# Performance work log

Measured on AMD Instinct MI355X. Metric: run time of the kernel, lower is better.

The kernel has to match this reference:

```python
import jax, jax.numpy as jnp
import numpy as np

EMBED_DIM = 1024
NUM_HEADS = 16
HEAD_DIM = EMBED_DIM // NUM_HEADS


def setup_inputs() -> dict:
    key = jax.random.key(0)
    k_x, k_wqkv, k_bqkv, k_wp, k_bp = jax.random.split(key, 5)
    B, S = 4, 2048
    scale = 1.0 / np.sqrt(EMBED_DIM)
    return {
        "x": jax.random.normal(k_x, (B, S, EMBED_DIM), dtype=jnp.float32),
        # torch nn.Linear stores weight as [out_features, in_features]
        "w_qkv": jax.random.uniform(k_wqkv, (3 * EMBED_DIM, EMBED_DIM), dtype=jnp.float32, minval=-scale, maxval=scale),
        "b_qkv": jax.random.uniform(k_bqkv, (3 * EMBED_DIM,), dtype=jnp.float32, minval=-scale, maxval=scale),
        "w_proj": jax.random.uniform(k_wp, (EMBED_DIM, EMBED_DIM), dtype=jnp.float32, minval=-scale, maxval=scale),
        "b_proj": jax.random.uniform(k_bp, (EMBED_DIM,), dtype=jnp.float32, minval=-scale, maxval=scale),
    }


def reference(x, w_qkv, b_qkv, w_proj, b_proj):
    B, S, _ = x.shape
    # qkv projection: [B,S,3E]
    qkv = jnp.einsum('bse,fe->bsf', x, w_qkv) + b_qkv
    qkv = qkv.reshape(B, S, 3, NUM_HEADS, HEAD_DIM)
    qkv = jnp.transpose(qkv, (2, 0, 3, 1, 4))  # [3,B,H,S,Dh]
    q, k, v = qkv[0], qkv[1], qkv[2]
    # scaled dot-product attention (no mask, eval-mode dropout = identity)
    scores = jnp.einsum('bhqd,bhkd->bhqk', q, k) / np.sqrt(HEAD_DIM)
    attn = jax.nn.softmax(scores, axis=-1)
    out = jnp.einsum('bhqk,bhkd->bhqd', attn, v)  # [B,H,S,Dh]
    out = jnp.transpose(out, (0, 2, 1, 3)).reshape(B, S, EMBED_DIM)
    return jnp.einsum('bse,fe->bsf', out, w_proj) + b_proj
```

## Files before the change

kernel.cpp:

```cpp
#include <hip/hip_runtime.h>

#define EDIM 1024
#define NHEADS 16
#define HDIM 64
#define SEQ 2048
#define BATCH 4
#define MROWS (BATCH * SEQ)
#define NQKV (3 * EDIM)
#define QKB 2048

typedef __attribute__((ext_vector_type(4))) float f32x4;
typedef __attribute__((ext_vector_type(8))) short s16x8;
typedef __attribute__((ext_vector_type(4))) short s16x4;
typedef __attribute__((ext_vector_type(4))) unsigned int u32x4;

#define AS1 __attribute__((address_space(1)))
#define AS3 __attribute__((address_space(3)))
#define GLOAD_LDS16(g, l) __builtin_amdgcn_global_load_lds( \
    (AS1 void*)(void*)(g), (AS3 void*)(void*)(l), 16, 0, 0)

static __device__ __forceinline__ unsigned short f2bf(float f) {
  unsigned int u = __builtin_bit_cast(unsigned int, f);
  u += 0x7fffu + ((u >> 16) & 1u);
  return (unsigned short)(u >> 16);
}

static __device__ __forceinline__ float fexp2(float x) {
  float r;
  asm("v_exp_f32 %0, %1" : "=v"(r) : "v"(x));
  return r;
}

static __device__ __forceinline__ unsigned int cvtpk(float a, float b) {
  unsigned int r;
  asm("v_cvt_pk_bf16_f32 %0, %1, %2" : "=v"(r) : "v"(a), "v"(b));
  return r;
}

static __device__ __forceinline__ f32x4 mfma_bf16(s16x8 a, s16x8 b, f32x4 c) {
  return __builtin_amdgcn_mfma_f32_16x16x32_bf16(a, b, c, 0, 0, 0);
}

__global__ void __launch_bounds__(256) cvt_all(const float* __restrict__ x,
                                               const float* __restrict__ wq,
                                               const float* __restrict__ wp,
                                               unsigned short* __restrict__ out) {
  const int i = blockIdx.x * 256 + threadIdx.x;
  const float* src;
  int j;
  if (i < 2097152) { src = x;  j = i; }
  else if (i < 2883584) { src = wq; j = i - 2097152; }
  else { src = wp; j = i - 2883584; }
  const float4 v = ((const float4*)src)[j];
  ushort4 o;
  o.x = f2bf(v.x); o.y = f2bf(v.y); o.z = f2bf(v.z); o.w = f2bf(v.w);
  ((ushort4*)out)[i] = o;
}

template <int MODE>
__global__ void __launch_bounds__(256) gemm_bt(const unsigned short* __restrict__ A,
                                               const unsigned short* __restrict__ B,
                                               const float* __restrict__ bias,
                                               void* __restrict__ Cout,
                                               int M, int N, int K) {
  __shared__ unsigned short As[128 * 32];
  __shared__ unsigned short Bs[128 * 32];
  const int tid = threadIdx.x;
  const int lane = tid & 63;
  const int wave = tid >> 6;
  const int wr = wave >> 1, wc = wave & 1;
  const int lr = lane & 15, kg = lane >> 4;

  const long m0 = (long)blockIdx.x * 128;
  const long n0 = (long)blockIdx.y * 128;

  f32x4 acc[4][4] = {};

  for (int kt = 0; kt < K; kt += 32) {
#pragma unroll
    for (int i = 0; i < 2; ++i) {
      const int c = wave + i * 4;
      const int slot = c * 64 + lane;
      const int row = slot >> 2;
      const int col = (slot & 3) << 3;
      GLOAD_LDS16(A + (m0 + row) * K + kt + col, &As[c * 512]);
      GLOAD_LDS16(B + (n0 + row) * K + kt + col, &Bs[c * 512]);
    }
    __syncthreads();

    s16x8 af[4], bf[4];
#pragma unroll
    for (int mt = 0; mt < 4; ++mt)
      af[mt] = *(const s16x8*)&As[(wr * 64 + mt * 16 + lr) * 32 + kg * 8];
#pragma unroll
    for (int nt = 0; nt < 4; ++nt)
      bf[nt] = *(const s16x8*)&Bs[(wc * 64 + nt * 16 + lr) * 32 + kg * 8];
#pragma unroll
    for (int mt = 0; mt < 4; ++mt)
#pragma unroll
      for (int nt = 0; nt < 4; ++nt)
        acc[mt][nt] = mfma_bf16(af[mt], bf[nt], acc[mt][nt]);
    __syncthreads();
  }

#pragma unroll
  for (int nt = 0; nt < 4; ++nt) {
    const long col = n0 + wc * 64 + nt * 16 + lr;
    const float bv = (MODE == 2) ? 0.f : bias[col];
#pragma unroll
    for (int mt = 0; mt < 4; ++mt) {
#pragma unroll
      for (int r = 0; r < 4; ++r) {
        const long row = m0 + wr * 64 + mt * 16 + kg * 4 + r;
        if (MODE == 0) {
          float v = acc[mt][nt][r] + bv;
          if (col < EDIM) v *= 0.18033688011112042f;
          ((unsigned short*)Cout)[row * N + col] = f2bf(v);
        } else if (MODE == 1) {
          ((float*)Cout)[row * N + col] = acc[mt][nt][r] + bv;
        } else {
          const float v = acc[mt][nt][r] + bias[row];
          ((unsigned short*)Cout)[(col >> 11) * (long)(1024 * 2048) +
                                  row * 2048 + (col & 2047)] = f2bf(v);
        }
      }
    }
  }
}

template <int BUF>
static __device__ __forceinline__ void attn_tile(
    const unsigned short (&Ks)[2][2][4096],
    const unsigned short (&Vs)[2][2][4096],
    const s16x8 (&qf)[2][2],
    f32x4 (&o_acc)[2][4],
    f32x4 (&l_part)[2],
    const int lr, const int kg) {
  unsigned int pk[2][2][4][2];
#pragma unroll
  for (int hh = 0; hh < 2; ++hh) {
    f32x4 st[2][4];
    __builtin_amdgcn_s_setprio(1);
#pragma unroll
    for (int ct = 0; ct < 4; ++ct) {
      const int rb = (ct * 16 + lr) * 128;
      const int sw = (lr & 7) << 4;
      const s16x8 k0 = *(const s16x8*)&Ks[BUF][hh][(rb + ((kg * 16) ^ sw)) >> 1];
      const s16x8 k1 = *(const s16x8*)&Ks[BUF][hh][(rb + ((64 + kg * 16) ^ sw)) >> 1];
#pragma unroll
      for (int qs = 0; qs < 2; ++qs) {
        f32x4 a = {};
        a = mfma_bf16(k0, qf[qs][0], a);
        a = mfma_bf16(k1, qf[qs][1], a);
        st[qs][ct] = a;
      }
    }
    __builtin_amdgcn_s_setprio(0);
#pragma unroll
    for (int qs = 0; qs < 2; ++qs) {
      f32x4 rv = {0.f, 0.f, 0.f, 0.f};
#pragma unroll
      for (int ct = 0; ct < 4; ++ct) {
        f32x4 p;
#pragma unroll
        for (int r = 0; r < 4; ++r) p[r] = fexp2(st[qs][ct][r]);
        rv += p;
        pk[qs][hh][ct][0] = cvtpk(p[0], p[1]);
        pk[qs][hh][ct][1] = cvtpk(p[2], p[3]);
      }
      l_part[qs] += rv;
    }
  }
#pragma unroll
  for (int hh = 0; hh < 2; ++hh) {
#pragma unroll
    for (int kc = 0; kc < 2; ++kc) {
      s16x8 pa[2];
#pragma unroll
      for (int qs = 0; qs < 2; ++qs) {
        u32x4 wv = {pk[qs][hh][2 * kc][0], pk[qs][hh][2 * kc][1],
                    pk[qs][hh][2 * kc + 1][0], pk[qs][hh][2 * kc + 1][1]};
        pa[qs] = __builtin_bit_cast(s16x8, wv);
      }
      __builtin_amdgcn_s_setprio(1);
#pragma unroll
      for (int dt = 0; dt < 4; ++dt) {
        const int rb = (dt * 16 + lr) * 128;
        const int c0 = (64 * kc + 8 * kg) ^ ((lr & 7) << 4);
        const s16x4 v0 = *(const s16x4*)&Vs[BUF][hh][(rb + c0) >> 1];
        const s16x4 v1 = *(const s16x4*)&Vs[BUF][hh][(rb + (c0 ^ 32)) >> 1];
        const s16x8 vf = __builtin_shufflevector(v0, v1, 0, 1, 2, 3, 4, 5, 6, 7);
#pragma unroll
        for (int qs = 0; qs < 2; ++qs)
          o_acc[qs][dt] = mfma_bf16(pa[qs], vf, o_acc[qs][dt]);
      }
      __builtin_amdgcn_s_setprio(0);
    }
  }
}

__global__ void __launch_bounds__(256, 2) attn_fwd(const unsigned short* __restrict__ qk,
                                                   const unsigned short* __restrict__ vT,
                                                   unsigned short* __restrict__ attout) {
  const int L = blockIdx.x;
  const int bh = (L & 7) * 8 + ((L >> 3) >> 4);
  const int qt = (L >> 3) & 15;
  const int b = bh >> 4, h = bh & 15;
  const int q0 = qt * 128;
  const int tid = threadIdx.x, lane = tid & 63, wave = tid >> 6;
  const int lr = lane & 15, kg = lane >> 4;

  __shared__ unsigned short Ks[2][2][4096];
  __shared__ unsigned short Vs[2][2][4096];

  const long rowbase = (long)b * SEQ;

#define STAGE(BUF, kv0) do {                                                     \
    _Pragma("unroll")                                                            \
    for (int hh_ = 0; hh_ < 2; ++hh_) {                                          \
      _Pragma("unroll")                                                          \
      for (int i_ = 0; i_ < 2; ++i_) {                                           \
        const int c_ = wave * 2 + i_;                                            \
        const int row_ = c_ * 8 + (lane >> 3);                                   \
        const int col_ = ((lane & 7) ^ (lane >> 3)) << 3;                        \
        GLOAD_LDS16(qk + (rowbase + (kv0) + hh_ * 64 + row_) * QKB + EDIM +      \
                        h * HDIM + col_,                                         \
                    &Ks[BUF][hh_][c_ * 512]);                                    \
        GLOAD_LDS16(vT + ((long)bh * HDIM + row_) * SEQ + (kv0) + hh_ * 64 +     \
                        col_,                                                    \
                    &Vs[BUF][hh_][c_ * 512]);                                    \
      }                                                                          \
    }                                                                            \
  } while (0)

  s16x8 qf[2][2];
#pragma unroll
  for (int qs = 0; qs < 2; ++qs) {
    const unsigned short* qp =
        qk + (rowbase + q0 + wave * 32 + qs * 16 + lr) * QKB + h * HDIM + kg * 8;
    qf[qs][0] = *(const s16x8*)qp;
    qf[qs][1] = *(const s16x8*)(qp + 32);
  }

  f32x4 l_part[2] = {{0.f, 0.f, 0.f, 0.f}, {0.f, 0.f, 0.f, 0.f}};
  f32x4 o_acc[2][4] = {};

  STAGE(0, 0);
  __syncthreads();

  for (int kv0 = 0; kv0 < SEQ; kv0 += 256) {
    STAGE(1, kv0 + 128);
    attn_tile<0>(Ks, Vs, qf, o_acc, l_part, lr, kg);
    __syncthreads();
    if (kv0 + 256 < SEQ) STAGE(0, kv0 + 256);
    attn_tile<1>(Ks, Vs, qf, o_acc, l_part, lr, kg);
    __syncthreads();
  }

#pragma unroll
  for (int qs = 0; qs < 2; ++qs) {
    float rs = (l_part[qs][0] + l_part[qs][1]) + (l_part[qs][2] + l_part[qs][3]);
    rs += __shfl_xor(rs, 16, 64);
    rs += __shfl_xor(rs, 32, 64);
#pragma unroll
    for (int r = 0; r < 4; ++r) {
      const float lq = __shfl(rs, kg * 4 + r, 64);
      const float inv = 1.0f / lq;
      const long row = rowbase + q0 + wave * 32 + qs * 16 + kg * 4 + r;
#pragma unroll
      for (int dt = 0; dt < 4; ++dt)
        attout[row * EDIM + h * HDIM + dt * 16 + lr] = f2bf(o_acc[qs][dt][r] * inv);
    }
  }
#undef STAGE
}

extern "C" void kernel_launch(void* const* d_in, const int* in_sizes, int n_in,
                              void* d_out, int out_size, void* d_ws, size_t ws_size,
                              hipStream_t stream) {
  const float* x      = (const float*)d_in[0];
  const float* w_qkv  = (const float*)d_in[1];
  const float* b_qkv  = (const float*)d_in[2];
  const float* w_proj = (const float*)d_in[3];
  const float* b_proj = (const float*)d_in[4];

  unsigned short* xb   = (unsigned short*)d_ws;
  unsigned short* wqb  = xb   + (size_t)MROWS * EDIM;
  unsigned short* wpb  = wqb  + (size_t)NQKV * EDIM;
  unsigned short* qkb  = wpb  + (size_t)EDIM * EDIM;
  unsigned short* attb = qkb  + (size_t)MROWS * QKB;
  unsigned short* vTb  = attb + (size_t)MROWS * EDIM;

  cvt_all<<<12288, 256, 0, stream>>>(x, w_qkv, w_proj, xb);

  gemm_bt<0><<<dim3(MROWS / 128, QKB / 128), 256, 0, stream>>>(
      xb, wqb, b_qkv, qkb, MROWS, QKB, EDIM);

  gemm_bt<2><<<dim3(EDIM / 128, MROWS / 128), 256, 0, stream>>>(
      wqb + (size_t)2048 * EDIM, xb, b_qkv + 2048, vTb, EDIM, MROWS, EDIM);

  attn_fwd<<<1024, 256, 0, stream>>>(qkb, vTb, attb);

  gemm_bt<1><<<dim3(MROWS / 128, EDIM / 128), 256, 0, stream>>>(
      attb, wpb, b_proj, d_out, MROWS, EDIM, EDIM);
}
```

Before: 210.4 us.

## Replace 128x128 GEMM with 256x256 tile, 4-stage LDS pipeline, swizzle, XCD remap

The GEMM is rewritten to use 256x256 output tiles with 512 threads (8 waves, each computing 128x64). It keeps a 4-deep ring of global-to-LDS async loads with explicit vmcnt waits, so loads overlap the MFMA work instead of synchronizing twice per k-step. LDS columns are XOR-swizzled to reduce bank conflicts, MFMA priority is raised, and block IDs are remapped across the 8 XCDs for better L2 locality. In exchange it uses 128KB of dynamic LDS and more accumulator registers, and it launches fewer workgroups, which could limit occupancy and leave some CUs idle.

```diff
diff --git a/kernel.cpp b/kernel.cpp
--- a/kernel.cpp
+++ b/kernel.cpp
@@ -58,49 +58,81 @@
 }
 
 template <int MODE>
-__global__ void __launch_bounds__(256) gemm_bt(const unsigned short* __restrict__ A,
-                                               const unsigned short* __restrict__ B,
-                                               const float* __restrict__ bias,
-                                               void* __restrict__ Cout,
-                                               int M, int N, int K) {
-  __shared__ unsigned short As[128 * 32];
-  __shared__ unsigned short Bs[128 * 32];
+__global__ void __launch_bounds__(512, 2) gemm256(const unsigned short* __restrict__ Ap,
+                                                  const unsigned short* __restrict__ Bp,
+                                                  const float* __restrict__ bias,
+                                                  void* __restrict__ Cout,
+                                                  int M, int N, int K) {
+  extern __shared__ unsigned short lds[];
   const int tid = threadIdx.x;
   const int lane = tid & 63;
   const int wave = tid >> 6;
-  const int wr = wave >> 1, wc = wave & 1;
+  const int wr = wave >> 2;
+  const int wc = wave & 3;
   const int lr = lane & 15, kg = lane >> 4;
 
-  const long m0 = (long)blockIdx.x * 128;
-  const long n0 = (long)blockIdx.y * 128;
-
-  f32x4 acc[4][4] = {};
-
-  for (int kt = 0; kt < K; kt += 32) {
-#pragma unroll
-    for (int i = 0; i < 2; ++i) {
-      const int c = wave + i * 4;
-      const int slot = c * 64 + lane;
-      const int row = slot >> 2;
-      const int col = (slot & 3) << 3;
-      GLOAD_LDS16(A + (m0 + row) * K + kt + col, &As[c * 512]);
-      GLOAD_LDS16(B + (n0 + row) * K + kt + col, &Bs[c * 512]);
-    }
-    __syncthreads();
-
-    s16x8 af[4], bf[4];
-#pragma unroll
-    for (int mt = 0; mt < 4; ++mt)
-      af[mt] = *(const s16x8*)&As[(wr * 64 + mt * 16 + lr) * 32 + kg * 8];
-#pragma unroll
-    for (int nt = 0; nt < 4; ++nt)
-      bf[nt] = *(const s16x8*)&Bs[(wc * 64 + nt * 16 + lr) * 32 + kg * 8];
-#pragma unroll
-    for (int mt = 0; mt < 4; ++mt)
+  const int nwg = gridDim.x;
+  const int q8 = nwg >> 3;
+  const int wgid = (blockIdx.x & 7) * q8 + (blockIdx.x >> 3);
+  const int NBM = M >> 8;
+  const long m0 = (long)(wgid % NBM) * 256;
+  const long n0 = (long)(wgid / NBM) * 256;
+
+#define STAGE(slot, kt) do {                                                   \
+    _Pragma("unroll")                                                          \
+    for (int i_ = 0; i_ < 2; ++i_) {                                           \
+      const int c_ = wave * 2 + i_;                     \
+      const int r_ = c_ * 16 + (lane >> 2);               \
+      const int sc_ = ((lane & 3) ^ ((r_ >> 1) & 3)) * 8;                      \
+      GLOAD_LDS16(Ap + (m0 + r_) * K + (kt) * 32 + sc_,                        \
+                  &lds[(slot) * 8192 + c_ * 512]);                             \
+      GLOAD_LDS16(Bp + (n0 + r_) * K + (kt) * 32 + sc_,                        \
+                  &lds[32768 + (slot) * 8192 + c_ * 512]);                     \
+    }                                                                          \
+  } while (0)
+
+  f32x4 acc[8][4] = {};
+  const int nk = K >> 5;
+
+  STAGE(0, 0); STAGE(1, 1); STAGE(2, 2);
+  asm volatile("s_waitcnt vmcnt(8)" ::: "memory");
+  __builtin_amdgcn_s_barrier();
+  __builtin_amdgcn_sched_barrier(0);
+
+  for (int t = 0; t < nk; ++t) {
+    if (t + 3 < nk) STAGE((t + 3) & 3, t + 3);
+
+    const unsigned short* Asl = &lds[(t & 3) * 8192];
+    const unsigned short* Bsl = &lds[32768 + (t & 3) * 8192];
+    s16x8 af[8], bf[4];
+#pragma unroll
+    for (int mt = 0; mt < 8; ++mt) {
+      const int r = wr * 128 + mt * 16 + lr;
+      af[mt] = *(const s16x8*)&Asl[r * 32 + ((kg * 8) ^ (((r >> 1) & 3) << 3))];
+    }
+#pragma unroll
+    for (int nt = 0; nt < 4; ++nt) {
+      const int r = wc * 64 + nt * 16 + lr;
+      bf[nt] = *(const s16x8*)&Bsl[r * 32 + ((kg * 8) ^ (((r >> 1) & 3) << 3))];
+    }
+    __builtin_amdgcn_s_setprio(1);
+#pragma unroll
+    for (int mt = 0; mt < 8; ++mt)
 #pragma unroll
       for (int nt = 0; nt < 4; ++nt)
         acc[mt][nt] = mfma_bf16(af[mt], bf[nt], acc[mt][nt]);
-    __syncthreads();
+    __builtin_amdgcn_s_setprio(0);
+
+    if (t + 1 < nk) {
+      if (t + 3 < nk)
+        asm volatile("s_waitcnt lgkmcnt(0) vmcnt(8)" ::: "memory");
+      else if (t + 2 < nk)
+        asm volatile("s_waitcnt lgkmcnt(0) vmcnt(4)" ::: "memory");
+      else
+        asm volatile("s_waitcnt lgkmcnt(0) vmcnt(0)" ::: "memory");
+      __builtin_amdgcn_s_barrier();
+      __builtin_amdgcn_sched_barrier(0);
+    }
   }
 
 #pragma unroll
@@ -108,24 +140,25 @@
     const long col = n0 + wc * 64 + nt * 16 + lr;
     const float bv = (MODE == 2) ? 0.f : bias[col];
 #pragma unroll
-    for (int mt = 0; mt < 4; ++mt) {
+    for (int mt = 0; mt < 8; ++mt) {
 #pragma unroll
       for (int r = 0; r < 4; ++r) {
-        const long row = m0 + wr * 64 + mt * 16 + kg * 4 + r;
+        const long row = m0 + wr * 128 + mt * 16 + kg * 4 + r;
         if (MODE == 0) {
           float v = acc[mt][nt][r] + bv;
           if (col < EDIM) v *= 0.18033688011112042f;
-          ((unsigned short*)Cout)[row * N + col] = f2bf(v);
+          ((unsigned short*)Cout)[row * QKB + col] = f2bf(v);
         } else if (MODE == 1) {
           ((float*)Cout)[row * N + col] = acc[mt][nt][r] + bv;
         } else {
           const float v = acc[mt][nt][r] + bias[row];
-          ((unsigned short*)Cout)[(col >> 11) * (long)(1024 * 2048) +
-                                  row * 2048 + (col & 2047)] = f2bf(v);
+          ((unsigned short*)Cout)[((col >> 11) * 1024 + row) * (long)2048 +
+                                  (col & 2047)] = f2bf(v);
         }
       }
     }
   }
+#undef STAGE
 }
 
 template <int BUF>
@@ -291,16 +324,24 @@
   unsigned short* attb = qkb  + (size_t)MROWS * QKB;
   unsigned short* vTb  = attb + (size_t)MROWS * EDIM;
 
+  const int shmem = 131072;
+  hipFuncSetAttribute((const void*)gemm256<0>,
+                      hipFuncAttributeMaxDynamicSharedMemorySize, shmem);
+  hipFuncSetAttribute((const void*)gemm256<1>,
+                      hipFuncAttributeMaxDynamicSharedMemorySize, shmem);
+  hipFuncSetAttribute((const void*)gemm256<2>,
+                      hipFuncAttributeMaxDynamicSharedMemorySize, shmem);
+
   cvt_all<<<12288, 256, 0, stream>>>(x, w_qkv, w_proj, xb);
 
-  gemm_bt<0><<<dim3(MROWS / 128, QKB / 128), 256, 0, stream>>>(
+  gemm256<0><<<(MROWS / 256) * (QKB / 256), 512, shmem, stream>>>(
       xb, wqb, b_qkv, qkb, MROWS, QKB, EDIM);
 
-  gemm_bt<2><<<dim3(EDIM / 128, MROWS / 128), 256, 0, stream>>>(
+  gemm256<2><<<(EDIM / 256) * (MROWS / 256), 512, shmem, stream>>>(
       wqb + (size_t)2048 * EDIM, xb, b_qkv + 2048, vTb, EDIM, MROWS, EDIM);
 
   attn_fwd<<<1024, 256, 0, stream>>>(qkb, vTb, attb);
 
-  gemm_bt<1><<<dim3(MROWS / 128, EDIM / 128), 256, 0, stream>>>(
+  gemm256<1><<<(MROWS / 256) * (EDIM / 256), 512, shmem, stream>>>(
       attb, wpb, b_proj, d_out, MROWS, EDIM, EDIM);
 }
```

Measured after the change: 208.0 us. About the same (-1.2%).
